# Optimization experiments

Hardware: AMD Instinct MI355X
Metric: run time of the kernel (lower is better)

The kernel has to match this reference:

```python
import jax, jax.numpy as jnp
import numpy as np

QMIN, QMAX = 0.0, 255.0  # uint8 affine quantization range


def _quant_dequant(x, scale, zero_point):
    # affine static quantization: q = clamp(round(x/scale) + zp, 0, 255)
    q = jnp.clip(jnp.round(x / scale) + zero_point, QMIN, QMAX)
    # dequantize back to float for the reference GEMM
    return (q - zero_point) * scale


def setup_inputs() -> dict:
    key = jax.random.key(0)
    k1, k2, k3, k4, k5 = jax.random.split(key, 5)
    N, IN, OUT = 4096, 4096, 4096
    x = jax.random.normal(k1, (N, IN), dtype=jnp.float32)
    weight = jax.random.normal(k2, (OUT, IN), dtype=jnp.float32) * 0.02
    bias = jax.random.normal(k3, (OUT,), dtype=jnp.float32)
    # static qparams (as produced by calculate_qparams of the observers)
    act_scale = jnp.float32(4.0 * 2.0 / 255.0)  # covers ~[-4, 4]
    act_zero_point = jnp.int32(128)
    weight_scale = (jax.random.uniform(k4, (OUT,), dtype=jnp.float32) * 0.5 + 0.5) * (0.08 * 2.0 / 255.0)
    weight_zero_point = jnp.full((OUT,), 128, dtype=jnp.int32)
    return {
        "x": x,
        "weight": weight,
        "bias": bias,
        "act_scale": act_scale,
        "act_zero_point": act_zero_point,
        "weight_scale": weight_scale,
        "weight_zero_point": weight_zero_point,
    }


def reference(x, weight, bias, act_scale, act_zero_point, weight_scale, weight_zero_point):
    # per-tensor static activation quantization
    x_dq = _quant_dequant(x, act_scale, act_zero_point.astype(jnp.float32))  # [N, in]
    # per-output-row weight quantization (block_size = (1, in_features))
    w_dq = _quant_dequant(
        weight,
        weight_scale[:, None],
        weight_zero_point.astype(jnp.float32)[:, None],
    )  # [out, in]
    # F.linear: x @ W^T + b
    return jnp.einsum("ni,oi->no", x_dq, w_dq) + bias
```

## Files before the change

### kernel.cpp

```cpp
#include <hip/hip_runtime.h>
#include <stdint.h>

typedef int   int4v   __attribute__((ext_vector_type(4)));
typedef float float4v __attribute__((ext_vector_type(4)));

static constexpr int DIM = 4096;
static constexpr int BM  = 256, BN = 256;
static constexpr int BK  = 128;
static constexpr int NKT = DIM / BK;

__global__ __launch_bounds__(256) void quant_act_kernel(
    const float* __restrict__ x, const float* __restrict__ s_ptr,
    const int* __restrict__ zp_ptr, int* __restrict__ out, int n4) {
  const float s  = s_ptr[0];
  const int   zp = zp_ptr[0];
  int idx    = blockIdx.x * blockDim.x + threadIdx.x;
  int stride = gridDim.x * blockDim.x;
  for (int i = idx; i < n4; i += stride) {
    float4v v = reinterpret_cast<const float4v*>(x)[i];
    int packed = 0;
#pragma unroll
    for (int j = 0; j < 4; ++j) {
      int q = (int)rintf(v[j] / s) + zp;
      q = min(max(q, 0), 255);
      q -= zp;
      packed |= (q & 255) << (8 * j);
    }
    out[i] = packed;
  }
}

__global__ __launch_bounds__(256) void quant_wgt_kernel(
    const float* __restrict__ w, const float* __restrict__ ws,
    const int* __restrict__ wzp, int* __restrict__ out, int n4) {
  int idx    = blockIdx.x * blockDim.x + threadIdx.x;
  int stride = gridDim.x * blockDim.x;
  for (int i = idx; i < n4; i += stride) {
    const int row = i >> 10;
    const float s = ws[row];
    const int  zp = wzp[row];
    float4v v = reinterpret_cast<const float4v*>(w)[i];
    int packed = 0;
#pragma unroll
    for (int j = 0; j < 4; ++j) {
      int q = (int)rintf(v[j] / s) + zp;
      q = min(max(q, 0), 255);
      q -= zp;
      packed |= (q & 255) << (8 * j);
    }
    out[i] = packed;
  }
}


#define MFMA_QUAD(AF, MH, NL)                                                  \
  __builtin_amdgcn_s_setprio(1);                                               \
  _Pragma("unroll") for (int kk = 0; kk < 2; ++kk)                             \
  _Pragma("unroll") for (int m = 0; m < 4; ++m)                                \
  _Pragma("unroll") for (int n = 0; n < 2; ++n)                                \
      acc[(MH)*4 + m][(NL) + n] = __builtin_amdgcn_mfma_i32_16x16x64_i8(       \
          AF[m][kk], bf[(NL) + n][kk], acc[(MH)*4 + m][(NL) + n], 0, 0, 0);    \
  __builtin_amdgcn_s_setprio(0);

__global__ __launch_bounds__(512) void gemm_i8_m201(
    const signed char* __restrict__ A, const signed char* __restrict__ B,
    const float* __restrict__ s_act, const float* __restrict__ w_scale,
    const float* __restrict__ bias, float* __restrict__ C) {
  extern __shared__ signed char smem[];

  const int tid  = threadIdx.x;
  const int w    = tid >> 6;
  const int lane = tid & 63;
  const int wr = w >> 2, wc = w & 3;
  const int l15 = lane & 15, lhi = lane >> 4;
  const int swk = (l15 & 7) << 4;

  const int srow = lane >> 3;
  const int scol = ((lane & 7) ^ (lane >> 3)) << 4;

  const int tileM = blockIdx.y * BM;
  const int tileN = blockIdx.x * BN;

  auto stageA = [&](int i, int t) {
    signed char* dst = smem + (t & 1) * 65536;
    const int c = 4 * w + i;
    const size_t g = (size_t)(tileM + c * 8 + srow) * DIM + (size_t)t * BK + scol;
    __builtin_amdgcn_global_load_lds(
        (const __attribute__((address_space(1))) void*)(A + g),
        (__attribute__((address_space(3))) void*)(dst + c * 1024), 16, 0, 0);
  };
  auto stageB = [&](int i, int t) {
    signed char* dst = smem + (t & 1) * 65536 + 32768;
    const int c = 4 * w + i;
    const size_t g = (size_t)(tileN + c * 8 + srow) * DIM + (size_t)t * BK + scol;
    __builtin_amdgcn_global_load_lds(
        (const __attribute__((address_space(1))) void*)(B + g),
        (__attribute__((address_space(3))) void*)(dst + c * 1024), 16, 0, 0);
  };
  auto rdA = [&](const signed char* aL, int mh, int m, int kk) -> int4v {
    const int r = wr * 128 + (mh * 4 + m) * 16 + l15;
    return *(const int4v*)(aL + r * BK + ((kk * 64 + lhi * 16) ^ swk));
  };
  auto rdB = [&](const signed char* bL, int nidx, int kk) -> int4v {
    const int r = wc * 64 + nidx * 16 + l15;
    return *(const int4v*)(bL + r * BK + ((kk * 64 + lhi * 16) ^ swk));
  };

  int4v acc[8][4] = {};
  int4v afLo[4][2];
  int4v afHi[4][2];
  int4v bf[4][2];

#pragma unroll
  for (int i = 0; i < 4; ++i) { stageA(i, 0); stageB(i, 0); }
  stageA(0, 1); stageB(0, 1); stageA(1, 1); stageB(1, 1);
  asm volatile("s_waitcnt vmcnt(4)" ::: "memory");
  __builtin_amdgcn_s_barrier();

  for (int kt = 0; kt < NKT; ++kt) {
    const signed char* aC = smem + (kt & 1) * 65536;
    const signed char* bC = aC + 32768;
    const bool s1 = (kt + 1 < NKT);
    const bool s2 = (kt + 2 < NKT);

#pragma unroll
    for (int m = 0; m < 4; ++m) { afLo[m][0] = rdA(aC, 0, m, 0); afLo[m][1] = rdA(aC, 0, m, 1); }
#pragma unroll
    for (int n = 0; n < 2; ++n) { bf[n][0] = rdB(bC, n, 0); bf[n][1] = rdB(bC, n, 1); }
    if (s1) { stageA(2, kt + 1); stageB(2, kt + 1); }
    __builtin_amdgcn_s_barrier();
    asm volatile("s_waitcnt lgkmcnt(0)" ::: "memory");
    MFMA_QUAD(afLo, 0, 0)
    __builtin_amdgcn_s_barrier();

#pragma unroll
    for (int m = 0; m < 4; ++m) { afHi[m][0] = rdA(aC, 1, m, 0); afHi[m][1] = rdA(aC, 1, m, 1); }
#pragma unroll
    for (int n = 2; n < 4; ++n) { bf[n][0] = rdB(bC, n, 0); bf[n][1] = rdB(bC, n, 1); }
    if (s1) { stageA(3, kt + 1); stageB(3, kt + 1); }
    __builtin_amdgcn_s_barrier();
    asm volatile("s_waitcnt lgkmcnt(0)" ::: "memory");
    MFMA_QUAD(afLo, 0, 2)
    __builtin_amdgcn_s_barrier();

    if (s2) { stageA(0, kt + 2); stageB(0, kt + 2); }
    __builtin_amdgcn_s_barrier();
    MFMA_QUAD(afHi, 1, 0)
    __builtin_amdgcn_s_barrier();

    if (s2) { stageA(1, kt + 2); stageB(1, kt + 2); }
    __builtin_amdgcn_s_barrier();
    MFMA_QUAD(afHi, 1, 2)
    if (s2) {
      asm volatile("s_waitcnt vmcnt(4)" ::: "memory");
    } else {
      asm volatile("s_waitcnt vmcnt(0)" ::: "memory");
    }
    __builtin_amdgcn_s_barrier();
  }

  const float sa = s_act[0];
#pragma unroll
  for (int n = 0; n < 4; ++n) {
    const int col = tileN + wc * 64 + n * 16 + l15;
    const float sc = sa * w_scale[col];
    const float bs = bias[col];
#pragma unroll
    for (int m = 0; m < 8; ++m) {
      const int rbase = tileM + wr * 128 + m * 16 + lhi * 4;
#pragma unroll
      for (int j = 0; j < 4; ++j)
        C[(size_t)(rbase + j) * DIM + col] = (float)acc[m][n][j] * sc + bs;
    }
  }
}

extern "C" void kernel_launch(void* const* d_in, const int* in_sizes, int n_in,
                              void* d_out, int out_size, void* d_ws, size_t ws_size,
                              hipStream_t stream) {
  const float* x    = (const float*)d_in[0];
  const float* w    = (const float*)d_in[1];
  const float* bias = (const float*)d_in[2];
  const float* a_s  = (const float*)d_in[3];
  const int*   a_zp = (const int*)d_in[4];
  const float* w_s  = (const float*)d_in[5];
  const int*   w_zp = (const int*)d_in[6];
  float* out = (float*)d_out;

  signed char* a8 = (signed char*)d_ws;
  signed char* b8 = a8 + (size_t)DIM * DIM;

  const int n4 = DIM * DIM / 4;
  quant_act_kernel<<<2048, 256, 0, stream>>>(x, a_s, a_zp, (int*)a8, n4);
  quant_wgt_kernel<<<2048, 256, 0, stream>>>(w, w_s, w_zp, (int*)b8, n4);

  (void)hipFuncSetAttribute((const void*)gemm_i8_m201,
                            hipFuncAttributeMaxDynamicSharedMemorySize, 131072);
  dim3 grid(DIM / BN, DIM / BM);
  gemm_i8_m201<<<grid, 512, 131072, stream>>>(a8, b8, a_s, w_s, bias, out);
}
```

Baseline: 98.25 us.

## Switch int8 GEMM to 32x32x32 MFMA with restructured software pipeline

Replaces the 16x16x64 int8 MFMA tiling with 32x32x32 MFMA instructions and 16-wide accumulators, which halves the LDS fragment reads per output. The main loop is also restructured. The whole next k-tile is staged at once, two tiles ahead, and the next tile's A/B fragments are prefetched from LDS during the last MFMA group. Fewer barriers are used, with sched_barrier and lgkmcnt waits keeping LDS reads overlapped with MFMAs. The risks are higher register pressure from prefetched fragments and a different epilogue store pattern.

After: 115.3 us. 17.3% more time.

```diff
diff --git a/kernel.cpp b/kernel.cpp
--- a/kernel.cpp
+++ b/kernel.cpp
@@ -2,6 +2,7 @@
 #include <stdint.h>
 
 typedef int   int4v   __attribute__((ext_vector_type(4)));
+typedef int   int16v  __attribute__((ext_vector_type(16)));
 typedef float float4v __attribute__((ext_vector_type(4)));
 
 static constexpr int DIM = 4096;
@@ -53,16 +54,7 @@
 }
 
 
-#define MFMA_QUAD(AF, MH, NL)                                                  \
-  __builtin_amdgcn_s_setprio(1);                                               \
-  _Pragma("unroll") for (int kk = 0; kk < 2; ++kk)                             \
-  _Pragma("unroll") for (int m = 0; m < 4; ++m)                                \
-  _Pragma("unroll") for (int n = 0; n < 2; ++n)                                \
-      acc[(MH)*4 + m][(NL) + n] = __builtin_amdgcn_mfma_i32_16x16x64_i8(       \
-          AF[m][kk], bf[(NL) + n][kk], acc[(MH)*4 + m][(NL) + n], 0, 0, 0);    \
-  __builtin_amdgcn_s_setprio(0);
-
-__global__ __launch_bounds__(512) void gemm_i8_m201(
+__global__ __launch_bounds__(512) void gemm_i8_32x32(
     const signed char* __restrict__ A, const signed char* __restrict__ B,
     const float* __restrict__ s_act, const float* __restrict__ w_scale,
     const float* __restrict__ bias, float* __restrict__ C) {
@@ -72,8 +64,8 @@
   const int w    = tid >> 6;
   const int lane = tid & 63;
   const int wr = w >> 2, wc = w & 3;
-  const int l15 = lane & 15, lhi = lane >> 4;
-  const int swk = (l15 & 7) << 4;
+  const int row31 = lane & 31, khalf = lane >> 5;
+  const int swk = (row31 & 7) << 4;
 
   const int srow = lane >> 3;
   const int scol = ((lane & 7) ^ (lane >> 3)) << 4;
@@ -97,82 +89,112 @@
         (const __attribute__((address_space(1))) void*)(B + g),
         (__attribute__((address_space(3))) void*)(dst + c * 1024), 16, 0, 0);
   };
-  auto rdA = [&](const signed char* aL, int mh, int m, int kk) -> int4v {
-    const int r = wr * 128 + (mh * 4 + m) * 16 + l15;
-    return *(const int4v*)(aL + r * BK + ((kk * 64 + lhi * 16) ^ swk));
-  };
-  auto rdB = [&](const signed char* bL, int nidx, int kk) -> int4v {
-    const int r = wc * 64 + nidx * 16 + l15;
-    return *(const int4v*)(bL + r * BK + ((kk * 64 + lhi * 16) ^ swk));
-  };
-
-  int4v acc[8][4] = {};
-  int4v afLo[4][2];
-  int4v afHi[4][2];
-  int4v bf[4][2];
+  auto rdA32 = [&](const signed char* aL, int m, int ks) -> int4v {
+    const int r = wr * 128 + m * 32 + row31;
+    return *(const int4v*)(aL + r * BK + ((ks * 32 + khalf * 16) ^ swk));
+  };
+  auto rdB32 = [&](const signed char* bL, int n, int ks) -> int4v {
+    const int r = wc * 64 + n * 32 + row31;
+    return *(const int4v*)(bL + r * BK + ((ks * 32 + khalf * 16) ^ swk));
+  };
+
+  int16v acc[4][2] = {};
+  int4v af0[2][4];
+  int4v af1[2][4];
+  int4v bf[2][4];
+
+#define MFMA_PAIR(AF, MBASE, NH)                                               \
+  __builtin_amdgcn_s_setprio(1);                                               \
+  _Pragma("unroll") for (int ks = 0; ks < 4; ++ks)                             \
+  _Pragma("unroll") for (int mi = 0; mi < 2; ++mi)                             \
+      acc[(MBASE) + mi][NH] = __builtin_amdgcn_mfma_i32_32x32x32_i8(           \
+          AF[mi][ks], bf[NH][ks], acc[(MBASE) + mi][NH], 0, 0, 0);             \
+  __builtin_amdgcn_s_setprio(0);
 
 #pragma unroll
   for (int i = 0; i < 4; ++i) { stageA(i, 0); stageB(i, 0); }
-  stageA(0, 1); stageB(0, 1); stageA(1, 1); stageB(1, 1);
-  asm volatile("s_waitcnt vmcnt(4)" ::: "memory");
+#pragma unroll
+  for (int i = 0; i < 4; ++i) { stageA(i, 1); stageB(i, 1); }
+  asm volatile("s_waitcnt vmcnt(8)" ::: "memory");
   __builtin_amdgcn_s_barrier();
+  {
+    const signed char* a0 = smem;
+    const signed char* b0 = smem + 32768;
+#pragma unroll
+    for (int mi = 0; mi < 2; ++mi)
+#pragma unroll
+      for (int ks = 0; ks < 4; ++ks) af0[mi][ks] = rdA32(a0, mi, ks);
+#pragma unroll
+    for (int ks = 0; ks < 4; ++ks) bf[0][ks] = rdB32(b0, 0, ks);
+  }
 
   for (int kt = 0; kt < NKT; ++kt) {
     const signed char* aC = smem + (kt & 1) * 65536;
     const signed char* bC = aC + 32768;
+    const signed char* aN = smem + ((kt + 1) & 1) * 65536;
+    const signed char* bN = aN + 32768;
     const bool s1 = (kt + 1 < NKT);
     const bool s2 = (kt + 2 < NKT);
 
 #pragma unroll
-    for (int m = 0; m < 4; ++m) { afLo[m][0] = rdA(aC, 0, m, 0); afLo[m][1] = rdA(aC, 0, m, 1); }
-#pragma unroll
-    for (int n = 0; n < 2; ++n) { bf[n][0] = rdB(bC, n, 0); bf[n][1] = rdB(bC, n, 1); }
-    if (s1) { stageA(2, kt + 1); stageB(2, kt + 1); }
+    for (int ks = 0; ks < 4; ++ks) bf[1][ks] = rdB32(bC, 1, ks);
+    asm volatile("s_waitcnt lgkmcnt(4)" ::: "memory");
+    __builtin_amdgcn_sched_barrier(0);
+    MFMA_PAIR(af0, 0, 0)
+
+#pragma unroll
+    for (int mi = 0; mi < 2; ++mi)
+#pragma unroll
+      for (int ks = 0; ks < 4; ++ks) af1[mi][ks] = rdA32(aC, 2 + mi, ks);
+    asm volatile("s_waitcnt lgkmcnt(8)" ::: "memory");
+    __builtin_amdgcn_sched_barrier(0);
+    MFMA_PAIR(af0, 0, 1)
+
+    asm volatile("s_waitcnt lgkmcnt(0)" ::: "memory");
+    __builtin_amdgcn_sched_barrier(0);
     __builtin_amdgcn_s_barrier();
-    asm volatile("s_waitcnt lgkmcnt(0)" ::: "memory");
-    MFMA_QUAD(afLo, 0, 0)
-    __builtin_amdgcn_s_barrier();
-
-#pragma unroll
-    for (int m = 0; m < 4; ++m) { afHi[m][0] = rdA(aC, 1, m, 0); afHi[m][1] = rdA(aC, 1, m, 1); }
-#pragma unroll
-    for (int n = 2; n < 4; ++n) { bf[n][0] = rdB(bC, n, 0); bf[n][1] = rdB(bC, n, 1); }
-    if (s1) { stageA(3, kt + 1); stageB(3, kt + 1); }
-    __builtin_amdgcn_s_barrier();
-    asm volatile("s_waitcnt lgkmcnt(0)" ::: "memory");
-    MFMA_QUAD(afLo, 0, 2)
-    __builtin_amdgcn_s_barrier();
-
-    if (s2) { stageA(0, kt + 2); stageB(0, kt + 2); }
-    __builtin_amdgcn_s_barrier();
-    MFMA_QUAD(afHi, 1, 0)
-    __builtin_amdgcn_s_barrier();
-
-    if (s2) { stageA(1, kt + 2); stageB(1, kt + 2); }
-    __builtin_amdgcn_s_barrier();
-    MFMA_QUAD(afHi, 1, 2)
     if (s2) {
-      asm volatile("s_waitcnt vmcnt(4)" ::: "memory");
+#pragma unroll
+      for (int i = 0; i < 4; ++i) { stageA(i, kt + 2); stageB(i, kt + 2); }
+    }
+    __builtin_amdgcn_sched_barrier(0);
+    MFMA_PAIR(af1, 2, 0)
+
+    if (s2) {
+      asm volatile("s_waitcnt vmcnt(8)" ::: "memory");
     } else {
       asm volatile("s_waitcnt vmcnt(0)" ::: "memory");
     }
     __builtin_amdgcn_s_barrier();
+    if (s1) {
+#pragma unroll
+      for (int mi = 0; mi < 2; ++mi)
+#pragma unroll
+        for (int ks = 0; ks < 4; ++ks) af0[mi][ks] = rdA32(aN, mi, ks);
+#pragma unroll
+      for (int ks = 0; ks < 4; ++ks) bf[0][ks] = rdB32(bN, 0, ks);
+    }
+    __builtin_amdgcn_sched_barrier(0);
+    MFMA_PAIR(af1, 2, 1)
   }
 
   const float sa = s_act[0];
 #pragma unroll
-  for (int n = 0; n < 4; ++n) {
-    const int col = tileN + wc * 64 + n * 16 + l15;
+  for (int n = 0; n < 2; ++n) {
+    const int col = tileN + wc * 64 + n * 32 + row31;
     const float sc = sa * w_scale[col];
     const float bs = bias[col];
 #pragma unroll
-    for (int m = 0; m < 8; ++m) {
-      const int rbase = tileM + wr * 128 + m * 16 + lhi * 4;
-#pragma unroll
-      for (int j = 0; j < 4; ++j)
-        C[(size_t)(rbase + j) * DIM + col] = (float)acc[m][n][j] * sc + bs;
-    }
-  }
+    for (int m = 0; m < 4; ++m) {
+      const int rbase = tileM + wr * 128 + m * 32 + 4 * khalf;
+#pragma unroll
+      for (int reg = 0; reg < 16; ++reg) {
+        const int row = rbase + (reg & 3) + 8 * (reg >> 2);
+        C[(size_t)row * DIM + col] = (float)acc[m][n][reg] * sc + bs;
+      }
+    }
+  }
+#undef MFMA_PAIR
 }
 
 extern "C" void kernel_launch(void* const* d_in, const int* in_sizes, int n_in,
@@ -194,8 +216,8 @@
   quant_act_kernel<<<2048, 256, 0, stream>>>(x, a_s, a_zp, (int*)a8, n4);
   quant_wgt_kernel<<<2048, 256, 0, stream>>>(w, w_s, w_zp, (int*)b8, n4);
 
-  (void)hipFuncSetAttribute((const void*)gemm_i8_m201,
+  (void)hipFuncSetAttribute((const void*)gemm_i8_32x32,
                             hipFuncAttributeMaxDynamicSharedMemorySize, 131072);
   dim3 grid(DIM / BN, DIM / BM);
-  gemm_i8_m201<<<grid, 512, 131072, stream>>>(a8, b8, a_s, w_s, bias, out);
-}
+  gemm_i8_32x32<<<grid, 512, 131072, stream>>>(a8, b8, a_s, w_s, bias, out);
+}
```
